# Optimization experiments

Measured on AMD Instinct MI355X. Metric: run time of the kernel, lower is better.

Reference implementation:

```python
import jax, jax.numpy as jnp
import numpy as np

D_MODEL = 512
N_HEADS = 8
DEPTH = D_MODEL // N_HEADS
NEG_INF = -1000000000.0


def setup_inputs() -> dict:
    key = jax.random.key(0)
    ks = jax.random.split(key, 12)
    B, S = 4, 2048
    scale = 0.02
    return {
        "Q": jax.random.normal(ks[0], (B, S, D_MODEL), jnp.float32),
        "K": jax.random.normal(ks[1], (B, S, D_MODEL), jnp.float32),
        "V": jax.random.normal(ks[2], (B, S, D_MODEL), jnp.float32),
        "mask": jax.random.randint(ks[3], (B, S, S), 0, 2, jnp.int32),
        "Wq": jax.random.normal(ks[4], (D_MODEL, D_MODEL), jnp.float32) * scale,
        "bq": jnp.zeros((D_MODEL,), jnp.float32),
        "Wk": jax.random.normal(ks[5], (D_MODEL, D_MODEL), jnp.float32) * scale,
        "bk": jnp.zeros((D_MODEL,), jnp.float32),
        "Wv": jax.random.normal(ks[6], (D_MODEL, D_MODEL), jnp.float32) * scale,
        "bv": jnp.zeros((D_MODEL,), jnp.float32),
        "Wo": jax.random.normal(ks[7], (D_MODEL, D_MODEL), jnp.float32) * scale,
        "bo": jnp.zeros((D_MODEL,), jnp.float32),
    }


def _split_heads(x, B):
    # [B, S, d_model] -> [B, H, S, depth]
    S = x.shape[1]
    return x.reshape(B, S, N_HEADS, DEPTH).transpose(0, 2, 1, 3)


def reference(Q, K, V, mask, Wq, bq, Wk, bk, Wv, bv, Wo, bo):
    B, S, _ = Q.shape
    q = _split_heads(Q @ Wq + bq, B)  # [B,H,S,d]
    k = _split_heads(K @ Wk + bk, B)
    v = _split_heads(V @ Wv + bv, B)
    scores = jnp.einsum("bhqd,bhkd->bhqk", q, k) / jnp.sqrt(
        jnp.asarray(DEPTH, jnp.float32))
    m = mask[:, None, :, :]  # broadcast over heads: [B,1,S,S]
    scores = jnp.where(m == 0, jnp.asarray(NEG_INF, scores.dtype), scores)
    attn = jax.nn.softmax(scores, axis=-1)
    ctx = jnp.einsum("bhqk,bhkd->bhqd", attn, v)
    ctx = ctx.transpose(0, 2, 1, 3).reshape(B, S, D_MODEL)
    return ctx @ Wo + bo
```

## Files before the change

kernel.cpp:

```cpp
#include <hip/hip_runtime.h>
#include <hip/hip_bf16.h>
#include <stdint.h>

typedef unsigned short u16;
typedef unsigned int u32;
typedef unsigned long long u64;
using bf16x8 = __attribute__((ext_vector_type(8))) __bf16;
using f32x4  = __attribute__((ext_vector_type(4))) float;
using f32x16 = __attribute__((ext_vector_type(16))) float;

static constexpr int B_ = 4, H_ = 8, S_ = 2048, D_ = 64, DM_ = 512;
#define QSCALE 0.1803368801111601f

__device__ __forceinline__ u16 f2b(float f) {
  u32 u = __float_as_uint(f);
  u = (u + 0x7FFFu + ((u >> 16) & 1u)) >> 16;
  return (u16)u;
}

__device__ __forceinline__ u32 cvtpk_bf16(float a, float b) {
  u32 r;
  asm("v_cvt_pk_bf16_f32 %0, %1, %2" : "=v"(r) : "v"(a), "v"(b));
  return r;
}
__device__ __forceinline__ void plswap(u32& a, u32& b) {
  asm("v_permlane32_swap_b32 %0, %1" : "+v"(a), "+v"(b));
}
__device__ __forceinline__ void gload16(const void* g, void* lds) {
  __builtin_amdgcn_global_load_lds(
      (const __attribute__((address_space(1))) u32*)g,
      (__attribute__((address_space(3))) u32*)lds, 16, 0, 0);
}
#if __has_builtin(__builtin_amdgcn_exp2f)
__device__ __forceinline__ float exp2fast(float x) { return __builtin_amdgcn_exp2f(x); }
#else
__device__ __forceinline__ float exp2fast(float x) {
  float r;
  asm("v_exp_f32 %0, %1" : "=v"(r) : "v"(x));
  return r;
}
#endif
__device__ __forceinline__ float selmask(float ex, u64 pred) {
  float r;
  asm("v_cndmask_b32 %0, 0, %1, %2" : "=v"(r) : "v"(ex), "s"(pred));
  return r;
}

__global__ __launch_bounds__(256) void prep_w_kernel(
    const float* __restrict__ Wq, const float* __restrict__ Wk,
    const float* __restrict__ Wv, const float* __restrict__ Wo,
    u16* __restrict__ Wtq, u16* __restrict__ Wtk, u16* __restrict__ Wtv, u16* __restrict__ Wto) {
  __shared__ float tile[32][33];
  const int z = blockIdx.z;
  const float* W = z == 0 ? Wq : z == 1 ? Wk : z == 2 ? Wv : Wo;
  u16* Wt       = z == 0 ? Wtq : z == 1 ? Wtk : z == 2 ? Wtv : Wto;
  const int k0 = blockIdx.x * 32, n0 = blockIdx.y * 32;
  const int t = threadIdx.x;
  {
    const int kl = t >> 3, nl4 = (t & 7) * 4;
    float4 v = *(const float4*)(W + (size_t)(k0 + kl) * DM_ + n0 + nl4);
    tile[kl][nl4 + 0] = v.x; tile[kl][nl4 + 1] = v.y;
    tile[kl][nl4 + 2] = v.z; tile[kl][nl4 + 3] = v.w;
  }
  __syncthreads();
  {
    const int nl = t >> 3, kl4 = (t & 7) * 4;
    ushort4 o;
    o.x = f2b(tile[kl4 + 0][nl]); o.y = f2b(tile[kl4 + 1][nl]);
    o.z = f2b(tile[kl4 + 2][nl]); o.w = f2b(tile[kl4 + 3][nl]);
    *(ushort4*)(Wt + (size_t)(n0 + nl) * DM_ + k0 + kl4) = o;
  }
}

__global__ __launch_bounds__(256) void pack_mask_kernel(const int* __restrict__ mask,
                                                        u64* __restrict__ wmask) {
  __shared__ int mt[4][32][65];
  const int t = threadIdx.x, lane = t & 63, w = t >> 6;
  const int kt = blockIdx.x * 4 + w, qg = blockIdx.y, b = blockIdx.z;
  const int q0 = qg * 32;
  const int* src = mask + ((size_t)b * S_ + q0) * S_ + kt * 64 + lane;
#pragma unroll 8
  for (int i = 0; i < 32; ++i) mt[w][i][lane] = src[(size_t)i * S_];
  u64* dst = wmask + (((size_t)(b * 64 + qg) * 32 + kt) * 32);
  const int hi4 = (lane >> 5) * 4;
#pragma unroll
  for (int idx = 0; idx < 32; ++idx) {
    const int ksub = idx >> 4, r = idx & 15;
    const int key = ksub * 32 + (r & 3) + 8 * (r >> 2) + hi4;
    u64 bal = __ballot(mt[w][lane & 31][key] != 0);
    if (lane == 0) dst[idx] = bal;
  }
}

__global__ __launch_bounds__(256) void gemm_qkv_kernel(
    const float* __restrict__ Qf, const float* __restrict__ Kf, const float* __restrict__ Vf,
    const u16* __restrict__ Wtq, const u16* __restrict__ Wtk, const u16* __restrict__ Wtv,
    const float* __restrict__ bq, const float* __restrict__ bk, const float* __restrict__ bv,
    u16* __restrict__ qp, u16* __restrict__ kp, u16* __restrict__ vp) {
  __shared__ __align__(16) float As[128 * 32];
  __shared__ __align__(16) u16  Bs[128 * 32];
  const int z = blockIdx.z;
  const float* A    = z == 0 ? Qf : z == 1 ? Kf : Vf;
  const u16* Bt     = z == 0 ? Wtq : z == 1 ? Wtk : Wtv;
  const float* bias = z == 0 ? bq : z == 1 ? bk : bv;
  u16* outp         = z == 0 ? qp : z == 1 ? kp : vp;
  const float scale = z == 0 ? QSCALE : 1.0f;

  const int t = threadIdx.x;
  const int lane = t & 63, wid = t >> 6;
  const int wr = wid >> 1, wc = wid & 1;
  const int l15 = lane & 15, l4 = lane >> 4;
  const int cn = blockIdx.x * 128, rm = blockIdx.y * 128;

  const int arow = t >> 3, acol = (t & 7) * 4;
  const float* asrc = A + (size_t)(rm + arow) * DM_ + acol;
  char* adst = (char*)As + wid * 1024;
  const int brow = t >> 2, bcol = (t & 3) * 8;
  const u16* bsrc = Bt + (size_t)(cn + brow) * DM_ + bcol;
  char* bdst = (char*)Bs + wid * 1024;

  f32x4 acc[4][4] = {};

  for (int k0 = 0; k0 < DM_; k0 += 32) {
    __syncthreads();
#pragma unroll
    for (int i = 0; i < 4; ++i)
      gload16(asrc + (size_t)(i * 32) * DM_ + k0, adst + i * 4096);
    gload16(bsrc + k0, bdst);
    gload16(bsrc + (size_t)64 * DM_ + k0, bdst + 4096);
    __syncthreads();
    bf16x8 af[4], bfr[4];
#pragma unroll
    for (int m = 0; m < 4; ++m) {
      const float* ap = As + (wr * 64 + m * 16 + l15) * 32 + l4 * 8;
      float4 x = *(const float4*)ap, y = *(const float4*)(ap + 4);
      union { u32 wds[4]; bf16x8 v; } c;
      c.wds[0] = cvtpk_bf16(x.x, x.y); c.wds[1] = cvtpk_bf16(x.z, x.w);
      c.wds[2] = cvtpk_bf16(y.x, y.y); c.wds[3] = cvtpk_bf16(y.z, y.w);
      af[m] = c.v;
    }
#pragma unroll
    for (int n = 0; n < 4; ++n)
      bfr[n] = *(const bf16x8*)((const char*)Bs + (wc * 64 + n * 16 + l15) * 64 + l4 * 16);
#pragma unroll
    for (int m = 0; m < 4; ++m)
#pragma unroll
      for (int n = 0; n < 4; ++n)
        acc[m][n] = __builtin_amdgcn_mfma_f32_16x16x32_bf16(af[m], bfr[n], acc[m][n], 0, 0, 0);
  }

#pragma unroll
  for (int m = 0; m < 4; ++m)
#pragma unroll
    for (int n = 0; n < 4; ++n) {
      int col = cn + wc * 64 + n * 16 + l15;
      float bv_ = bias[col];
#pragma unroll
      for (int r = 0; r < 4; ++r) {
        int row = rm + wr * 64 + m * 16 + l4 * 4 + r;
        float v = (acc[m][n][r] + bv_) * scale;
        int b = row >> 11, s = row & 2047;
        int h = col >> 6, d = col & 63;
        if (z < 2)
          outp[(((size_t)(b * H_ + h)) * S_ + s) * D_ + d] = f2b(v);
        else
          outp[(((size_t)(b * H_ + h)) * D_ + d) * S_ + s] = f2b(v);
      }
    }
}

__global__ __launch_bounds__(256) void gemm_out_kernel(
    const u16* __restrict__ A, const u16* __restrict__ Bt,
    const float* __restrict__ bias, float* __restrict__ outp) {
  __shared__ __align__(16) u16 As[64 * 32];
  __shared__ __align__(16) u16 Bs[128 * 32];
  const int t = threadIdx.x;
  const int lane = t & 63, w = t >> 6;
  const int l15 = lane & 15, l4 = lane >> 4;
  const int cn = blockIdx.x * 128, rm = blockIdx.y * 64;

  const int srow = w * 16 + (lane >> 2), scol = (lane & 3) * 8;
  const u16* asrc = A + (size_t)(rm + srow) * DM_ + scol;
  const u16* bsrc = Bt + (size_t)(cn + srow) * DM_ + scol;
  char* adst = (char*)As + w * 1024;
  char* bdst = (char*)Bs + w * 1024;

  f32x4 acc[4][2] = {};

  for (int k0 = 0; k0 < DM_; k0 += 32) {
    __syncthreads();
    gload16(asrc + k0, adst);
    gload16(bsrc + k0, bdst);
    gload16(bsrc + (size_t)64 * DM_ + k0, bdst + 4096);
    __syncthreads();
    bf16x8 af[4], bfr[2];
#pragma unroll
    for (int m = 0; m < 4; ++m)
      af[m] = *(const bf16x8*)((const char*)As + (m * 16 + l15) * 64 + l4 * 16);
#pragma unroll
    for (int n = 0; n < 2; ++n)
      bfr[n] = *(const bf16x8*)((const char*)Bs + (w * 32 + n * 16 + l15) * 64 + l4 * 16);
#pragma unroll
    for (int m = 0; m < 4; ++m)
#pragma unroll
      for (int n = 0; n < 2; ++n)
        acc[m][n] = __builtin_amdgcn_mfma_f32_16x16x32_bf16(af[m], bfr[n], acc[m][n], 0, 0, 0);
  }

#pragma unroll
  for (int m = 0; m < 4; ++m)
#pragma unroll
    for (int n = 0; n < 2; ++n) {
      int col = cn + w * 32 + n * 16 + l15;
      float bv_ = bias[col];
#pragma unroll
      for (int r = 0; r < 4; ++r) {
        int row = rm + m * 16 + l4 * 4 + r;
        outp[(size_t)row * DM_ + col] = acc[m][n][r] + bv_;
      }
    }
}

__global__ __launch_bounds__(256, 3) void attn_kernel(
    const u16* __restrict__ qp, const u16* __restrict__ kp, const u16* __restrict__ vp,
    const u64* __restrict__ wmask, u16* __restrict__ ctx) {
  __shared__ __align__(16) char smem[49152];
  const int t = threadIdx.x, lane = t & 63, w = t >> 6;
  const int l31 = lane & 31, hi = lane >> 5;
  const int ksub = w & 1, qsub = w >> 1;
  const int wu = __builtin_amdgcn_readfirstlane(w);
  const int wgid = blockIdx.x;
  const int h = wgid & 7, idx = wgid >> 3;
  const int b = idx >> 5, qt = idx & 31;
  const size_t head  = ((size_t)(b * H_ + h)) * S_ * D_;
  const size_t headT = ((size_t)(b * H_ + h)) * D_ * S_;
  const int q0 = qt * 64 + qsub * 32;
  const int q  = q0 + l31;

  bf16x8 qf[4];
  {
    const u16* qrow = qp + head + (size_t)q * D_;
#pragma unroll
    for (int ks = 0; ks < 4; ++ks) qf[ks] = *(const bf16x8*)(qrow + ks * 16 + hi * 8);
  }

  const u64* wm = wmask + (((size_t)(b * 64 + qt * 2 + (wu >> 1)) * 32) * 32) + (wu & 1) * 16;

  const int kxor = (l31 & 7) << 4;
  const int krbase = (ksub * 32 + l31) * 128;
  const int rbase0 = l31 * 128, rbase1 = (32 + l31) * 128;
  int colx[4];
#pragma unroll
  for (int s = 0; s < 4; ++s) colx[s] = ((s * 32 + hi * 16) ^ kxor);
  int vcolx[2];
#pragma unroll
  for (int s = 0; s < 2; ++s) vcolx[s] = ((ksub * 64 + s * 32 + hi * 16) ^ kxor);

  const int srow = lane >> 3;
  const int scol = ((lane & 7) ^ srow) << 3;
  const int c0 = w, c1 = w + 4;
  const u16* ksrc0 = kp + head + (size_t)(c0 * 8 + srow) * D_ + scol;
  const u16* ksrc1 = kp + head + (size_t)(c1 * 8 + srow) * D_ + scol;
  const u16* vsrc0 = vp + headT + (size_t)(c0 * 8 + srow) * S_ + scol;
  const u16* vsrc1 = vp + headT + (size_t)(c1 * 8 + srow) * S_ + scol;

  f32x16 accO0, accO1, lacc, FZ;
#pragma unroll
  for (int i = 0; i < 16; ++i) { accO0[i] = 0.f; accO1[i] = 0.f; lacc[i] = 0.f; FZ[i] = 0.f; }
  union { u32 wds[4]; bf16x8 v; } ones;
#pragma unroll
  for (int i = 0; i < 4; ++i) ones.wds[i] = 0x3F803F80u;

  auto stage = [&](int bufi, int kt) {
    char* kb = smem + bufi * 16384;
    char* vb = kb + 8192;
    gload16(ksrc0 + (size_t)kt * 4096, kb + c0 * 1024);
    gload16(ksrc1 + (size_t)kt * 4096, kb + c1 * 1024);
    gload16(vsrc0 + kt * 64, vb + c0 * 1024);
    gload16(vsrc1 + kt * 64, vb + c1 * 1024);
  };

  constexpr int NT = S_ / 64;
  stage(0, 0);
  stage(1, 1);
  u64 mskr[16];
#pragma unroll
  for (int r = 0; r < 16; ++r) mskr[r] = wm[r];
  asm volatile("s_waitcnt vmcnt(4)" ::: "memory");
  __builtin_amdgcn_s_barrier();
  asm volatile("" ::: "memory");

  for (int kt = 0; kt < NT; ++kt) {
    const int cur = kt % 3;
    if (kt < NT - 2) stage((kt + 2) % 3, kt + 2);

    const char* kb = smem + cur * 16384;
    const char* vb = kb + 8192;

    f32x16 s;
    {
      bf16x8 kf[4];
#pragma unroll
      for (int ks = 0; ks < 4; ++ks) kf[ks] = *(const bf16x8*)(kb + krbase + colx[ks]);
      __builtin_amdgcn_s_setprio(1);
      s = __builtin_amdgcn_mfma_f32_32x32x16_bf16(kf[0], qf[0], FZ, 0, 0, 0);
#pragma unroll
      for (int ks = 1; ks < 4; ++ks)
        s = __builtin_amdgcn_mfma_f32_32x32x16_bf16(kf[ks], qf[ks], s, 0, 0, 0);
      __builtin_amdgcn_s_setprio(0);
    }

    float e[16];
#pragma unroll
    for (int r = 0; r < 16; ++r) e[r] = selmask(exp2fast(s[r]), mskr[r]);

    {
      u32 pw[8];
#pragma unroll
      for (int j = 0; j < 8; ++j)
        pw[j] = cvtpk_bf16(e[2 * j], e[2 * j + 1]);
      plswap(pw[0], pw[2]); plswap(pw[1], pw[3]);
      plswap(pw[4], pw[6]); plswap(pw[5], pw[7]);
      __builtin_amdgcn_s_setprio(1);
#pragma unroll
      for (int s2 = 0; s2 < 2; ++s2) {
        union { u32 wds[4]; bf16x8 v; } pa;
        pa.wds[0] = pw[s2 * 4 + 0]; pa.wds[1] = pw[s2 * 4 + 1];
        pa.wds[2] = pw[s2 * 4 + 2]; pa.wds[3] = pw[s2 * 4 + 3];
        bf16x8 vf0 = *(const bf16x8*)(vb + rbase0 + vcolx[s2]);
        accO0 = __builtin_amdgcn_mfma_f32_32x32x16_bf16(pa.v, vf0, accO0, 0, 0, 0);
        bf16x8 vf1 = *(const bf16x8*)(vb + rbase1 + vcolx[s2]);
        accO1 = __builtin_amdgcn_mfma_f32_32x32x16_bf16(pa.v, vf1, accO1, 0, 0, 0);
        lacc = __builtin_amdgcn_mfma_f32_32x32x16_bf16(pa.v, ones.v, lacc, 0, 0, 0);
      }
      __builtin_amdgcn_s_setprio(0);
    }

    if (kt < NT - 1) {
      const u64* wmk = wm + (kt + 1) * 32;
#pragma unroll
      for (int r = 0; r < 16; ++r) mskr[r] = wmk[r];
    }

    if (kt < NT - 1) {
      if (kt < NT - 2) {
        asm volatile("s_waitcnt vmcnt(4)" ::: "memory");
      } else {
        asm volatile("s_waitcnt vmcnt(0)" ::: "memory");
      }
      __builtin_amdgcn_s_barrier();
      asm volatile("" ::: "memory");
    }
  }

  float (*Ol)[32][64] = (float (*)[32][64])smem;
  float (*La)[32] = (float (*)[32])(smem + 16384);
  if (ksub == 1) {
#pragma unroll
    for (int r = 0; r < 16; ++r) {
      const int qr = (r & 3) + 8 * (r >> 2) + 4 * hi;
      Ol[qsub][qr][l31]      = accO0[r];
      Ol[qsub][qr][32 + l31] = accO1[r];
      if (l31 == 0) La[qsub][qr] = lacc[r];
    }
  }
  __syncthreads();
  if (ksub == 0) {
    const int colA = h * 64 + l31, colB = h * 64 + 32 + l31;
#pragma unroll
    for (int r = 0; r < 16; ++r) {
      const int qr = (r & 3) + 8 * (r >> 2) + 4 * hi;
      const int row = q0 + qr;
      const float inv = 1.0f / (lacc[r] + La[qsub][qr]);
      u16* o = ctx + ((size_t)(b * S_) + row) * DM_;
      o[colA] = f2b((accO0[r] + Ol[qsub][qr][l31])      * inv);
      o[colB] = f2b((accO1[r] + Ol[qsub][qr][32 + l31]) * inv);
    }
  }
}

extern "C" void kernel_launch(void* const* d_in, const int* in_sizes, int n_in,
                              void* d_out, int out_size, void* d_ws, size_t ws_size,
                              hipStream_t stream) {
  const float* Q  = (const float*)d_in[0];
  const float* K  = (const float*)d_in[1];
  const float* V  = (const float*)d_in[2];
  const int* mask = (const int*)d_in[3];
  const float* Wq = (const float*)d_in[4];
  const float* bq = (const float*)d_in[5];
  const float* Wk = (const float*)d_in[6];
  const float* bk = (const float*)d_in[7];
  const float* Wv = (const float*)d_in[8];
  const float* bv = (const float*)d_in[9];
  const float* Wo = (const float*)d_in[10];
  const float* bo = (const float*)d_in[11];

  char* ws = (char*)d_ws;
  size_t off = 0;
  auto alloc = [&](size_t bytes) -> void* {
    void* p = ws + off;
    off += (bytes + 255) & ~(size_t)255;
    return p;
  };
  const size_t act_b = (size_t)B_ * S_ * DM_ * 2;
  u16* Wtq = (u16*)alloc((size_t)DM_ * DM_ * 2);
  u16* Wtk = (u16*)alloc((size_t)DM_ * DM_ * 2);
  u16* Wtv = (u16*)alloc((size_t)DM_ * DM_ * 2);
  u16* Wto = (u16*)alloc((size_t)DM_ * DM_ * 2);
  u64* wmask = (u64*)alloc((size_t)B_ * 64 * 32 * 32 * 8);
  u16* qp  = (u16*)alloc(act_b);
  u16* kp  = (u16*)alloc(act_b);
  u16* vp  = (u16*)alloc(act_b);
  u16* ctx = (u16*)alloc(act_b);

  prep_w_kernel<<<dim3(16, 16, 4), 256, 0, stream>>>(Wq, Wk, Wv, Wo, Wtq, Wtk, Wtv, Wto);
  pack_mask_kernel<<<dim3(8, 64, 4), 256, 0, stream>>>(mask, wmask);

  gemm_qkv_kernel<<<dim3(4, 64, 3), 256, 0, stream>>>(
      Q, K, V, Wtq, Wtk, Wtv, bq, bk, bv, qp, kp, vp);

  attn_kernel<<<dim3(1024), 256, 0, stream>>>(qp, kp, vp, wmask, ctx);

  gemm_out_kernel<<<dim3(4, 128), 256, 0, stream>>>(ctx, Wto, bo, (float*)d_out);
}
```

Before: 132.0 us.

## Merge mask packing into QKV GEMM launch; double-buffer attention with four-block occupancy

Merges the mask-packing work into the QKV projection kernel as extra blocks of a single 1D grid. Each mask block handles eight of the former mask tiles, so one launch is removed and the memory-bound packing runs alongside the GEMM blocks. The attention kernel moves from a triple-buffered K/V pipeline with hand-placed waitcnt and barriers to a double-buffered one using plain __syncthreads. This cuts its LDS footprint from 48KB to 32KB and raises launch bounds to allow four blocks per CU, at the cost of less prefetch depth and a full vmcnt(0) wait at each barrier.

Measured after the change: 135.1 us. +2.3%, slower.

```diff
diff --git a/kernel.cpp b/kernel.cpp
--- a/kernel.cpp
+++ b/kernel.cpp
@@ -72,45 +72,52 @@
   }
 }
 
-__global__ __launch_bounds__(256) void pack_mask_kernel(const int* __restrict__ mask,
-                                                        u64* __restrict__ wmask) {
-  __shared__ int mt[4][32][65];
-  const int t = threadIdx.x, lane = t & 63, w = t >> 6;
-  const int kt = blockIdx.x * 4 + w, qg = blockIdx.y, b = blockIdx.z;
-  const int q0 = qg * 32;
-  const int* src = mask + ((size_t)b * S_ + q0) * S_ + kt * 64 + lane;
-#pragma unroll 8
-  for (int i = 0; i < 32; ++i) mt[w][i][lane] = src[(size_t)i * S_];
-  u64* dst = wmask + (((size_t)(b * 64 + qg) * 32 + kt) * 32);
-  const int hi4 = (lane >> 5) * 4;
-#pragma unroll
-  for (int idx = 0; idx < 32; ++idx) {
-    const int ksub = idx >> 4, r = idx & 15;
-    const int key = ksub * 32 + (r & 3) + 8 * (r >> 2) + hi4;
-    u64 bal = __ballot(mt[w][lane & 31][key] != 0);
-    if (lane == 0) dst[idx] = bal;
-  }
-}
-
-__global__ __launch_bounds__(256) void gemm_qkv_kernel(
+__global__ __launch_bounds__(256) void qkv_pack_kernel(
     const float* __restrict__ Qf, const float* __restrict__ Kf, const float* __restrict__ Vf,
     const u16* __restrict__ Wtq, const u16* __restrict__ Wtk, const u16* __restrict__ Wtv,
     const float* __restrict__ bq, const float* __restrict__ bk, const float* __restrict__ bv,
-    u16* __restrict__ qp, u16* __restrict__ kp, u16* __restrict__ vp) {
-  __shared__ __align__(16) float As[128 * 32];
-  __shared__ __align__(16) u16  Bs[128 * 32];
-  const int z = blockIdx.z;
+    u16* __restrict__ qp, u16* __restrict__ kp, u16* __restrict__ vp,
+    const int* __restrict__ mask, u64* __restrict__ wmask) {
+  __shared__ __align__(16) char smem[33280];
+  const int g = blockIdx.x;
+  const int t = threadIdx.x;
+  const int lane = t & 63, wid = t >> 6;
+
+  if (g >= 768) {
+    int* mt = (int*)smem + wid * (32 * 65);
+    const int base = (g - 768) * 8;
+    for (int i = 0; i < 8; ++i) {
+      const int p = base + i;
+      const int x = p & 7, y = (p >> 3) & 63, z = p >> 9;
+      const int kt = x * 4 + wid, qg = y, b = z;
+      const int* src = mask + ((size_t)b * S_ + qg * 32) * S_ + kt * 64 + lane;
+#pragma unroll 8
+      for (int j = 0; j < 32; ++j) mt[j * 65 + lane] = src[(size_t)j * S_];
+      u64* dst = wmask + (((size_t)(b * 64 + qg) * 32 + kt) * 32);
+      const int hi4 = (lane >> 5) * 4;
+#pragma unroll
+      for (int idx = 0; idx < 32; ++idx) {
+        const int ksub = idx >> 4, r = idx & 15;
+        const int key = ksub * 32 + (r & 3) + 8 * (r >> 2) + hi4;
+        u64 bal = __ballot(mt[(lane & 31) * 65 + key] != 0);
+        if (lane == 0) dst[idx] = bal;
+      }
+    }
+    return;
+  }
+
+  float* As = (float*)smem;
+  u16*  Bs  = (u16*)(smem + 16384);
+  const int z = g >> 8, rem = g & 255;
   const float* A    = z == 0 ? Qf : z == 1 ? Kf : Vf;
   const u16* Bt     = z == 0 ? Wtq : z == 1 ? Wtk : Wtv;
   const float* bias = z == 0 ? bq : z == 1 ? bk : bv;
   u16* outp         = z == 0 ? qp : z == 1 ? kp : vp;
   const float scale = z == 0 ? QSCALE : 1.0f;
 
-  const int t = threadIdx.x;
-  const int lane = t & 63, wid = t >> 6;
   const int wr = wid >> 1, wc = wid & 1;
   const int l15 = lane & 15, l4 = lane >> 4;
-  const int cn = blockIdx.x * 128, rm = blockIdx.y * 128;
+  const int cn = (rem & 3) * 128, rm = (rem >> 2) * 128;
 
   const int arow = t >> 3, acol = (t & 7) * 4;
   const float* asrc = A + (size_t)(rm + arow) * DM_ + acol;
@@ -221,10 +228,10 @@
     }
 }
 
-__global__ __launch_bounds__(256, 3) void attn_kernel(
+__global__ __launch_bounds__(256, 4) void attn_kernel(
     const u16* __restrict__ qp, const u16* __restrict__ kp, const u16* __restrict__ vp,
     const u64* __restrict__ wmask, u16* __restrict__ ctx) {
-  __shared__ __align__(16) char smem[49152];
+  __shared__ __align__(16) char smem[32768];
   const int t = threadIdx.x, lane = t & 63, w = t >> 6;
   const int l31 = lane & 31, hi = lane >> 5;
   const int ksub = w & 1, qsub = w >> 1;
@@ -272,30 +279,26 @@
   for (int i = 0; i < 4; ++i) ones.wds[i] = 0x3F803F80u;
 
   auto stage = [&](int bufi, int kt) {
-    char* kb = smem + bufi * 16384;
-    char* vb = kb + 8192;
+    char* kb = smem + bufi * 8192;
+    char* vb = smem + 16384 + bufi * 8192;
     gload16(ksrc0 + (size_t)kt * 4096, kb + c0 * 1024);
     gload16(ksrc1 + (size_t)kt * 4096, kb + c1 * 1024);
     gload16(vsrc0 + kt * 64, vb + c0 * 1024);
     gload16(vsrc1 + kt * 64, vb + c1 * 1024);
   };
 
-  constexpr int NT = S_ / 64;
   stage(0, 0);
-  stage(1, 1);
   u64 mskr[16];
 #pragma unroll
   for (int r = 0; r < 16; ++r) mskr[r] = wm[r];
-  asm volatile("s_waitcnt vmcnt(4)" ::: "memory");
-  __builtin_amdgcn_s_barrier();
-  asm volatile("" ::: "memory");
-
-  for (int kt = 0; kt < NT; ++kt) {
-    const int cur = kt % 3;
-    if (kt < NT - 2) stage((kt + 2) % 3, kt + 2);
-
-    const char* kb = smem + cur * 16384;
-    const char* vb = kb + 8192;
+  __syncthreads();
+  int buf = 0;
+
+  for (int kt = 0; kt < S_ / 64; ++kt) {
+    if (kt < S_ / 64 - 1) stage(buf ^ 1, kt + 1);
+
+    const char* kb = smem + buf * 8192;
+    const char* vb = smem + 16384 + buf * 8192;
 
     f32x16 s;
     {
@@ -336,21 +339,13 @@
       __builtin_amdgcn_s_setprio(0);
     }
 
-    if (kt < NT - 1) {
+    if (kt < S_ / 64 - 1) {
       const u64* wmk = wm + (kt + 1) * 32;
 #pragma unroll
       for (int r = 0; r < 16; ++r) mskr[r] = wmk[r];
     }
-
-    if (kt < NT - 1) {
-      if (kt < NT - 2) {
-        asm volatile("s_waitcnt vmcnt(4)" ::: "memory");
-      } else {
-        asm volatile("s_waitcnt vmcnt(0)" ::: "memory");
-      }
-      __builtin_amdgcn_s_barrier();
-      asm volatile("" ::: "memory");
-    }
+    __syncthreads();
+    buf ^= 1;
   }
 
   float (*Ol)[32][64] = (float (*)[32][64])smem;
@@ -414,10 +409,9 @@
   u16* ctx = (u16*)alloc(act_b);
 
   prep_w_kernel<<<dim3(16, 16, 4), 256, 0, stream>>>(Wq, Wk, Wv, Wo, Wtq, Wtk, Wtv, Wto);
-  pack_mask_kernel<<<dim3(8, 64, 4), 256, 0, stream>>>(mask, wmask);
-
-  gemm_qkv_kernel<<<dim3(4, 64, 3), 256, 0, stream>>>(
-      Q, K, V, Wtq, Wtk, Wtv, bq, bk, bv, qp, kp, vp);
+
+  qkv_pack_kernel<<<dim3(1024), 256, 0, stream>>>(
+      Q, K, V, Wtq, Wtk, Wtv, bq, bk, bv, qp, kp, vp, mask, wmask);
 
   attn_kernel<<<dim3(1024), 256, 0, stream>>>(qp, kp, vp, wmask, ctx);
 
```
